# Kernel optimization log

Hardware: AMD Instinct MI355X
Metric: run time of the kernel (lower is better)

## Reference

```python
import jax, jax.numpy as jnp
import numpy as np
from jax import lax

B, CM, CQ, CO, H, W, KS = 8, 64, 64, 64, 128, 128, 3
K = KS * KS  # 9 kernel taps, offset_group=1


def setup_inputs() -> dict:
    key = jax.random.key(0)
    k1, k2, k3, k4 = jax.random.split(key, 4)
    mem = jax.random.normal(k1, (B, CM, H, W), jnp.float32)
    que = jax.random.normal(k2, (B, CQ, H, W), jnp.float32)
    # conv_offset: Conv2d(CM+CQ -> 3*K, 3x3, pad=1, bias=True); small init so offsets are a few px
    w_off = jax.random.normal(k3, (3 * K, CM + CQ, KS, KS), jnp.float32) * 0.01
    b_off = jnp.zeros((3 * K,), jnp.float32)
    # deformable conv weight: [CO, CM, 3, 3], bias=False
    w_def = jax.random.normal(k4, (CO, CM, KS, KS), jnp.float32) * (1.0 / np.sqrt(CM * K))
    return {"mem": mem, "que": que, "w_off": w_off, "b_off": b_off, "w_def": w_def}


def _deform_conv2d(mem, offset, mask, w_def):
    """Deformable conv v2 (stride=1, pad=1, dil=1, groups=1, offset_group=1).
    mem: [B,C,H,W]; offset: [B,2K,H,W] (dy,dx pairs per tap); mask: [B,K,H,W]."""
    Bn, C, Hn, Wn = mem.shape
    Kn = w_def.shape[2] * w_def.shape[3]
    off = offset.reshape(Bn, Kn, 2, Hn, Wn)
    dy, dx = off[:, :, 0], off[:, :, 1]            # [B,K,H,W]
    kk = jnp.arange(Kn)
    ky = (kk // KS - 1).astype(jnp.float32)        # kernel tap offsets with pad=1, dil=1
    kx = (kk % KS - 1).astype(jnp.float32)
    gy = jnp.arange(Hn, dtype=jnp.float32)
    gx = jnp.arange(Wn, dtype=jnp.float32)
    py = gy[None, None, :, None] + ky[None, :, None, None] + dy   # sample y coords [B,K,H,W]
    px = gx[None, None, None, :] + kx[None, :, None, None] + dx   # sample x coords [B,K,H,W]
    y0 = jnp.floor(py)
    x0 = jnp.floor(px)
    fy = py - y0
    fx = px - x0
    b_idx = jnp.arange(Bn)[:, None, None, None]

    def corner(iy, ix, wgt):
        valid = (iy >= 0) & (iy < Hn) & (ix >= 0) & (ix < Wn)  # zero padding outside
        iyc = jnp.clip(iy.astype(jnp.int32), 0, Hn - 1)
        ixc = jnp.clip(ix.astype(jnp.int32), 0, Wn - 1)
        vals = mem[b_idx, :, iyc, ixc]             # gather -> [B,K,H,W,C]
        return vals * (wgt * valid)[..., None]

    sampled = (corner(y0, x0, (1 - fy) * (1 - fx))
               + corner(y0, x0 + 1, (1 - fy) * fx)
               + corner(y0 + 1, x0, fy * (1 - fx))
               + corner(y0 + 1, x0 + 1, fy * fx))
    sampled = sampled * mask[..., None]            # modulation (applied raw, as in source)
    w = w_def.reshape(w_def.shape[0], C, Kn)       # [O,C,K]; tap order kh*KS+kw matches kk
    return jnp.einsum('bkhwc,ock->bohw', sampled, w)


def reference(mem, que, w_off, b_off, w_def):
    x = jnp.concatenate([mem, que], axis=1)
    off = lax.conv_general_dilated(
        x, w_off, window_strides=(1, 1), padding=[(1, 1), (1, 1)],
        dimension_numbers=('NCHW', 'OIHW', 'NCHW')) + b_off[None, :, None, None]
    offset, mask = off[:, :2 * K], off[:, 2 * K:]
    return _deform_conv2d(mem, offset, mask, w_def)
```

## Files before the change

kernel.cpp:

```cpp
#include <hip/hip_runtime.h>
#include <hip/hip_bf16.h>

#define Bn   8
#define CM_  64
#define CIN  128
#define CO_  64
#define Hn   128
#define Wn   128
#define Kn   9
#define COFF 27
#define HW   (Hn * Wn)

typedef __attribute__((ext_vector_type(8))) short bf16x8;
typedef __attribute__((ext_vector_type(4))) float f32x4;

__device__ __forceinline__ unsigned short f2bf(float x) {
    union { float f; unsigned u; } v; v.f = x;
    unsigned r = v.u + 0x7FFF + ((v.u >> 16) & 1);
    return (unsigned short)(r >> 16);
}
__device__ __forceinline__ float blo(unsigned u) {
    union { unsigned u; float f; } v; v.u = u << 16; return v.f;
}
__device__ __forceinline__ float bhi(unsigned u) {
    union { unsigned u; float f; } v; v.u = u & 0xffff0000u; return v.f;
}

__global__ __launch_bounds__(256) void transpose_kernel(
    const float* __restrict__ mem, const float* __restrict__ que,
    uint4* __restrict__ xT4)
{
    __shared__ unsigned tile[64 * 65];

    const int bb   = blockIdx.x & 7;
    const int pix0 = (blockIdx.x >> 3) * 64;
    const int tid  = threadIdx.x;
    const int pxL  = tid & 63;
    const int cg   = tid >> 6;

    const float* mb = mem + (size_t)bb * CM_ * HW + pix0 + pxL;
    const float* qb = que + (size_t)bb * CM_ * HW + pix0 + pxL;

    #pragma unroll
    for (int i = 0; i < 16; ++i) {
        const int c = cg * 32 + 2 * i;
        const float v0 = (c < CM_) ? mb[(size_t)c * HW]       : qb[(size_t)(c - CM_) * HW];
        const float v1 = (c + 1 < CM_) ? mb[(size_t)(c + 1) * HW] : qb[(size_t)(c + 1 - CM_) * HW];
        tile[pxL * 65 + cg * 16 + i] =
            (unsigned)f2bf(v0) | ((unsigned)f2bf(v1) << 16);
    }
    __syncthreads();

    uint4* dst = xT4 + (size_t)(bb * HW + pix0) * 16;
    #pragma unroll
    for (int p = 0; p < 4; ++p) {
        const int G  = p * 256 + tid;
        const int px = G >> 4;
        const int u  = G & 15;
        uint4 v;
        v.x = tile[px * 65 + u * 4 + 0];
        v.y = tile[px * 65 + u * 4 + 1];
        v.z = tile[px * 65 + u * 4 + 2];
        v.w = tile[px * 65 + u * 4 + 3];
        dst[G] = v;
    }
}

__global__ __launch_bounds__(256) void wprep_def_kernel(
    const float* __restrict__ w_def, unsigned short* __restrict__ wp)
{
    const int idx = blockIdx.x * 256 + threadIdx.x;
    if (idx >= CO_ * CM_ * Kn) return;
    const int j  = idx & 7;
    const int L  = (idx >> 3) & 63;
    const int f  = (idx >> 9) & 1;
    const int gk = idx >> 10;
    const int k  = gk % 9;
    const int g  = gk / 9;
    const int o  = g * 16 + (L & 15);
    const int c  = f * 32 + (L >> 4) * 8 + j;
    wp[idx] = f2bf(w_def[(size_t)(o * CM_ + c) * Kn + k]);
}

__global__ __launch_bounds__(256) void wprep_off_kernel(
    const float* __restrict__ w_off, unsigned short* __restrict__ wp)
{
    const int idx = blockIdx.x * 256 + threadIdx.x;
    if (idx >= 2 * 9 * 4 * 64 * 8) return;
    const int j   = idx & 7;
    const int L   = (idx >> 3) & 63;
    const int s   = (idx >> 9) & 3;
    const int r   = idx >> 11;
    const int tap = r % 9;
    const int ot  = r / 9;
    const int o   = ot * 16 + (L & 15);
    const int c   = s * 32 + (L >> 4) * 8 + j;
    wp[idx] = (o < COFF) ? f2bf(w_off[(size_t)(o * CIN + c) * Kn + tap]) : (unsigned short)0;
}

__global__ __launch_bounds__(256) void off_conv_mfma(
    const uint4* __restrict__ xT4, const uint4* __restrict__ wpo,
    const float* __restrict__ b_off, float* __restrict__ off)
{
    __shared__ uint4 xw[198 * 16];

    const int bb   = blockIdx.x & 7;
    const int pix0 = (blockIdx.x >> 3) * 64;
    const int h    = pix0 >> 7;
    const int w0   = pix0 & 127;
    const int tid  = threadIdx.x;
    const int wv   = tid >> 6;
    const int lane = tid & 63;
    const int quad = lane >> 4;
    const int lrow = lane & 15;
    const int ot   = wv >> 1;
    const int sub0 = (wv & 1) * 2;

    const uint4* xb = xT4 + (size_t)bb * HW * 16;

    #pragma unroll
    for (int g = 0; g < 13; ++g) {
        const int idx = g * 256 + tid;
        if (idx < 198 * 16) {
            const int slot = idx >> 4;
            const int j    = idx & 15;
            const int r    = slot / 66;
            const int c    = slot - r * 66;
            const int y    = h + r - 1;
            const int x    = w0 + c - 1;
            const bool ok  = (y >= 0) & (y < Hn) & (x >= 0) & (x < Wn);
            uint4 v = make_uint4(0, 0, 0, 0);
            if (ok) v = xb[(size_t)(y * Wn + x) * 16 + j];
            xw[slot * 16 + (j ^ (slot & 7))] = v;
        }
    }
    __syncthreads();

    f32x4 acc[2];
    #pragma unroll
    for (int t = 0; t < 2; ++t)
        #pragma unroll
        for (int r = 0; r < 4; ++r) {
            const int o = ot * 16 + quad * 4 + r;
            acc[t][r] = (o < COFF) ? b_off[o] : 0.0f;
        }

    #pragma unroll
    for (int tap = 0; tap < 9; ++tap) {
        const int rr = tap / 3;
        const int cc = tap % 3;

        const uint4* ap = wpo + (size_t)((ot * 9 + tap) * 4) * 64 + lane;
        bf16x8 a[4];
        #pragma unroll
        for (int s = 0; s < 4; ++s) a[s] = __builtin_bit_cast(bf16x8, ap[s * 64]);

        #pragma unroll
        for (int t = 0; t < 2; ++t) {
            const int pl   = (sub0 + t) * 16 + lrow;
            const int slot = rr * 66 + pl + cc;
            const int base = slot * 16;
            const int sw   = slot & 7;
            #pragma unroll
            for (int s = 0; s < 4; ++s) {
                const bf16x8 bfrag = __builtin_bit_cast(bf16x8,
                    xw[base + ((s * 4 + quad) ^ sw)]);
                acc[t] = __builtin_amdgcn_mfma_f32_16x16x32_bf16(
                    a[s], bfrag, acc[t], 0, 0, 0);
            }
        }
    }

    #pragma unroll
    for (int t = 0; t < 2; ++t) {
        const int pp = pix0 + (sub0 + t) * 16 + lrow;
        #pragma unroll
        for (int r = 0; r < 4; ++r) {
            const int o = ot * 16 + quad * 4 + r;
            if (o < COFF)
                off[(size_t)(bb * COFF + o) * HW + pp] = acc[t][r];
        }
    }
}

__global__ __launch_bounds__(256) void deform_mfma_kernel(
    const uint4* __restrict__ xT4, const float* __restrict__ off,
    const uint4* __restrict__ wprep, float* __restrict__ out)
{
    __shared__ uint4 smp4[64 * 8];

    const int bb    = blockIdx.x & 7;
    const int pix0  = (blockIdx.x >> 3) * 64;
    const int tid   = threadIdx.x;
    const int wv    = tid >> 6;
    const int lane  = tid & 63;
    const int quad  = lane >> 4;
    const int lrow  = lane & 15;
    const int chunk = lane & 7;
    const int psub  = lane >> 3;

    const uint4*  xb      = xT4 + (size_t)bb * HW * 16;
    const float*  offbase = off + (size_t)bb * COFF * HW;

    f32x4 acc[4];
    #pragma unroll
    for (int i = 0; i < 4; ++i) acc[i] = (f32x4){0.f, 0.f, 0.f, 0.f};

    for (int k = 0; k < Kn; ++k) {
        #pragma unroll
        for (int g = 0; g < 2; ++g) {
            const int pl = g * 32 + wv * 8 + psub;
            const int p  = pix0 + pl;
            const int h  = p >> 7;
            const int w  = p & 127;

            const float dy = offbase[(2 * k    ) * HW + p];
            const float dx = offbase[(2 * k + 1) * HW + p];
            const float mk = offbase[(18 + k   ) * HW + p];

            const float py = (float)(h + k / 3 - 1) + dy;
            const float px = (float)(w + k % 3 - 1) + dx;
            const float y0f = floorf(py), x0f = floorf(px);
            const float fy = py - y0f,  fx = px - x0f;
            const int y0 = (int)y0f, x0 = (int)x0f;
            const int y1 = y0 + 1,   x1 = x0 + 1;
            const bool vy0 = (y0 >= 0) & (y0 < Hn);
            const bool vy1 = (y1 >= 0) & (y1 < Hn);
            const bool vx0 = (x0 >= 0) & (x0 < Wn);
            const bool vx1 = (x1 >= 0) & (x1 < Wn);
            const float w00 = (1.f - fy) * (1.f - fx) * (float)(vy0 & vx0) * mk;
            const float w01 = (1.f - fy) * fx         * (float)(vy0 & vx1) * mk;
            const float w10 = fy * (1.f - fx)         * (float)(vy1 & vx0) * mk;
            const float w11 = fy * fx                 * (float)(vy1 & vx1) * mk;
            const int y0c = min(max(y0, 0), Hn - 1);
            const int y1c = min(max(y1, 0), Hn - 1);
            const int x0c = min(max(x0, 0), Wn - 1);
            const int x1c = min(max(x1, 0), Wn - 1);
            const int i00 = y0c * Wn + x0c, i01 = y0c * Wn + x1c;
            const int i10 = y1c * Wn + x0c, i11 = y1c * Wn + x1c;

            const uint4 v00 = xb[(size_t)i00 * 16 + chunk];
            const uint4 v01 = xb[(size_t)i01 * 16 + chunk];
            const uint4 v10 = xb[(size_t)i10 * 16 + chunk];
            const uint4 v11 = xb[(size_t)i11 * 16 + chunk];
            const unsigned u00[4] = {v00.x, v00.y, v00.z, v00.w};
            const unsigned u01[4] = {v01.x, v01.y, v01.z, v01.w};
            const unsigned u10[4] = {v10.x, v10.y, v10.z, v10.w};
            const unsigned u11[4] = {v11.x, v11.y, v11.z, v11.w};
            unsigned pk[4];
            #pragma unroll
            for (int d = 0; d < 4; ++d) {
                const float slo = w00 * blo(u00[d]) + w01 * blo(u01[d])
                                + w10 * blo(u10[d]) + w11 * blo(u11[d]);
                const float shi = w00 * bhi(u00[d]) + w01 * bhi(u01[d])
                                + w10 * bhi(u10[d]) + w11 * bhi(u11[d]);
                pk[d] = (unsigned)f2bf(slo) | ((unsigned)f2bf(shi) << 16);
            }
            smp4[pl * 8 + (chunk ^ (pl & 7))] =
                make_uint4(pk[0], pk[1], pk[2], pk[3]);
        }
        __syncthreads();

        const uint4* wpk = wprep + (size_t)((wv * 9 + k) * 2) * 64 + lane;
        const bf16x8 a0 = __builtin_bit_cast(bf16x8, wpk[0]);
        const bf16x8 a1 = __builtin_bit_cast(bf16x8, wpk[64]);

        #pragma unroll
        for (int nt = 0; nt < 4; ++nt) {
            const int pm = nt * 16 + lrow;
            const bf16x8 b0 = __builtin_bit_cast(bf16x8,
                smp4[pm * 8 + ( quad      ^ (pm & 7))]);
            const bf16x8 b1 = __builtin_bit_cast(bf16x8,
                smp4[pm * 8 + ((quad + 4) ^ (pm & 7))]);
            acc[nt] = __builtin_amdgcn_mfma_f32_16x16x32_bf16(a0, b0, acc[nt], 0, 0, 0);
            acc[nt] = __builtin_amdgcn_mfma_f32_16x16x32_bf16(a1, b1, acc[nt], 0, 0, 0);
        }
        __syncthreads();
    }

    const int obase = (wv << 4) + (quad << 2);
    #pragma unroll
    for (int nt = 0; nt < 4; ++nt) {
        const int pp = pix0 + nt * 16 + lrow;
        #pragma unroll
        for (int r = 0; r < 4; ++r)
            out[(size_t)(bb * CO_ + obase + r) * HW + pp] = acc[nt][r];
    }
}

extern "C" void kernel_launch(void* const* d_in, const int* in_sizes, int n_in,
                              void* d_out, int out_size, void* d_ws, size_t ws_size,
                              hipStream_t stream) {
    const float* mem   = (const float*)d_in[0];
    const float* que   = (const float*)d_in[1];
    const float* w_off = (const float*)d_in[2];
    const float* b_off = (const float*)d_in[3];
    const float* w_def = (const float*)d_in[4];
    float* out = (float*)d_out;

    char* ws = (char*)d_ws;
    float*          off  = (float*)ws;
    unsigned short* wpd  = (unsigned short*)(ws + 14155776);
    unsigned short* wpo  = (unsigned short*)(ws + 14229504);
    uint4*          xT4  = (uint4*)(ws + 14303232);

    transpose_kernel<<<2048, 256, 0, stream>>>(mem, que, xT4);
    wprep_def_kernel<<<144, 256, 0, stream>>>(w_def, wpd);
    wprep_off_kernel<<<144, 256, 0, stream>>>(w_off, wpo);
    off_conv_mfma<<<2048, 256, 0, stream>>>(xT4, (const uint4*)wpo, b_off, off);
    deform_mfma_kernel<<<2048, 256, 0, stream>>>(xT4, off, (const uint4*)wpd, out);
}
```

Measured before the change: 195.3 us.

## Double-buffer sample tile, prefetch next tap gathers, share offset math via shuffles

Doubles the shared sampling tile so the next tap's gathers are issued before the current tap's MFMAs, and the blend and write happen afterwards into the alternate buffer. This removes one barrier per tap and hides gather latency behind matrix work. Per-pixel offset and bilinear weight math is now done once per lane and broadcast with shuffles instead of being recomputed by all 8 chunk lanes. The blend uses packed float2 math and a library bf16x2 conversion. In exchange, register pressure rises from holding the prefetched gathers, and shared memory use doubles.

```diff
diff --git a/kernel.cpp b/kernel.cpp
--- a/kernel.cpp
+++ b/kernel.cpp
@@ -13,6 +13,7 @@
 
 typedef __attribute__((ext_vector_type(8))) short bf16x8;
 typedef __attribute__((ext_vector_type(4))) float f32x4;
+typedef __attribute__((ext_vector_type(2))) float f32x2;
 
 __device__ __forceinline__ unsigned short f2bf(float x) {
     union { float f; unsigned u; } v; v.f = x;
@@ -24,6 +25,12 @@
 }
 __device__ __forceinline__ float bhi(unsigned u) {
     union { unsigned u; float f; } v; v.u = u & 0xffff0000u; return v.f;
+}
+__device__ __forceinline__ unsigned pack_bf2(float lo, float hi) {
+    __hip_bfloat162 r = __float22bfloat162_rn(make_float2(lo, hi));
+    unsigned u;
+    __builtin_memcpy(&u, &r, 4);
+    return u;
 }
 
 __global__ __launch_bounds__(256) void transpose_kernel(
@@ -187,7 +194,7 @@
     const uint4* __restrict__ xT4, const float* __restrict__ off,
     const uint4* __restrict__ wprep, float* __restrict__ out)
 {
-    __shared__ uint4 smp4[64 * 8];
+    __shared__ uint4 smp4[2][64 * 8];
 
     const int bb    = blockIdx.x & 7;
     const int pix0  = (blockIdx.x >> 3) * 64;
@@ -202,64 +209,93 @@
     const uint4*  xb      = xT4 + (size_t)bb * HW * 16;
     const float*  offbase = off + (size_t)bb * COFF * HW;
 
+    const int pM = pix0 + lane;
+    const int hM = pM >> 7;
+    const int wM = pM & 127;
+
     f32x4 acc[4];
     #pragma unroll
     for (int i = 0; i < 4; ++i) acc[i] = (f32x4){0.f, 0.f, 0.f, 0.f};
 
-    for (int k = 0; k < Kn; ++k) {
+    float W00[2], W01[2], W10[2], W11[2];
+    uint4 G00[2], G01[2], G10[2], G11[2];
+
+    auto prep = [&](int k) {
+        const float dy = offbase[(2 * k    ) * HW + pM];
+        const float dx = offbase[(2 * k + 1) * HW + pM];
+        const float mk = offbase[(18 + k   ) * HW + pM];
+        const float py = (float)(hM + k / 3 - 1) + dy;
+        const float px = (float)(wM + k % 3 - 1) + dx;
+        const float y0f = floorf(py), x0f = floorf(px);
+        const float fy = py - y0f,  fx = px - x0f;
+        const int y0 = (int)y0f, x0 = (int)x0f;
+        const int y1 = y0 + 1,   x1 = x0 + 1;
+        const bool vy0 = (y0 >= 0) & (y0 < Hn);
+        const bool vy1 = (y1 >= 0) & (y1 < Hn);
+        const bool vx0 = (x0 >= 0) & (x0 < Wn);
+        const bool vx1 = (x1 >= 0) & (x1 < Wn);
+        const float w00 = (1.f - fy) * (1.f - fx) * (float)(vy0 & vx0) * mk;
+        const float w01 = (1.f - fy) * fx         * (float)(vy0 & vx1) * mk;
+        const float w10 = fy * (1.f - fx)         * (float)(vy1 & vx0) * mk;
+        const float w11 = fy * fx                 * (float)(vy1 & vx1) * mk;
+        const int y0c = min(max(y0, 0), Hn - 1);
+        const int y1c = min(max(y1, 0), Hn - 1);
+        const int x0c = min(max(x0, 0), Wn - 1);
+        const int x1c = min(max(x1, 0), Wn - 1);
+        const int i00 = y0c * Wn + x0c, i01 = y0c * Wn + x1c;
+        const int i10 = y1c * Wn + x0c, i11 = y1c * Wn + x1c;
+
         #pragma unroll
         for (int g = 0; g < 2; ++g) {
             const int pl = g * 32 + wv * 8 + psub;
-            const int p  = pix0 + pl;
-            const int h  = p >> 7;
-            const int w  = p & 127;
-
-            const float dy = offbase[(2 * k    ) * HW + p];
-            const float dx = offbase[(2 * k + 1) * HW + p];
-            const float mk = offbase[(18 + k   ) * HW + p];
-
-            const float py = (float)(h + k / 3 - 1) + dy;
-            const float px = (float)(w + k % 3 - 1) + dx;
-            const float y0f = floorf(py), x0f = floorf(px);
-            const float fy = py - y0f,  fx = px - x0f;
-            const int y0 = (int)y0f, x0 = (int)x0f;
-            const int y1 = y0 + 1,   x1 = x0 + 1;
-            const bool vy0 = (y0 >= 0) & (y0 < Hn);
-            const bool vy1 = (y1 >= 0) & (y1 < Hn);
-            const bool vx0 = (x0 >= 0) & (x0 < Wn);
-            const bool vx1 = (x1 >= 0) & (x1 < Wn);
-            const float w00 = (1.f - fy) * (1.f - fx) * (float)(vy0 & vx0) * mk;
-            const float w01 = (1.f - fy) * fx         * (float)(vy0 & vx1) * mk;
-            const float w10 = fy * (1.f - fx)         * (float)(vy1 & vx0) * mk;
-            const float w11 = fy * fx                 * (float)(vy1 & vx1) * mk;
-            const int y0c = min(max(y0, 0), Hn - 1);
-            const int y1c = min(max(y1, 0), Hn - 1);
-            const int x0c = min(max(x0, 0), Wn - 1);
-            const int x1c = min(max(x1, 0), Wn - 1);
-            const int i00 = y0c * Wn + x0c, i01 = y0c * Wn + x1c;
-            const int i10 = y1c * Wn + x0c, i11 = y1c * Wn + x1c;
-
-            const uint4 v00 = xb[(size_t)i00 * 16 + chunk];
-            const uint4 v01 = xb[(size_t)i01 * 16 + chunk];
-            const uint4 v10 = xb[(size_t)i10 * 16 + chunk];
-            const uint4 v11 = xb[(size_t)i11 * 16 + chunk];
-            const unsigned u00[4] = {v00.x, v00.y, v00.z, v00.w};
-            const unsigned u01[4] = {v01.x, v01.y, v01.z, v01.w};
-            const unsigned u10[4] = {v10.x, v10.y, v10.z, v10.w};
-            const unsigned u11[4] = {v11.x, v11.y, v11.z, v11.w};
+            W00[g] = __shfl(w00, pl, 64);
+            W01[g] = __shfl(w01, pl, 64);
+            W10[g] = __shfl(w10, pl, 64);
+            W11[g] = __shfl(w11, pl, 64);
+            const int I00 = __shfl(i00, pl, 64);
+            const int I01 = __shfl(i01, pl, 64);
+            const int I10 = __shfl(i10, pl, 64);
+            const int I11 = __shfl(i11, pl, 64);
+            G00[g] = xb[(size_t)I00 * 16 + chunk];
+            G01[g] = xb[(size_t)I01 * 16 + chunk];
+            G10[g] = xb[(size_t)I10 * 16 + chunk];
+            G11[g] = xb[(size_t)I11 * 16 + chunk];
+        }
+    };
+
+    auto blendwrite = [&](int buf) {
+        #pragma unroll
+        for (int g = 0; g < 2; ++g) {
+            const int pl = g * 32 + wv * 8 + psub;
+            const unsigned u00[4] = {G00[g].x, G00[g].y, G00[g].z, G00[g].w};
+            const unsigned u01[4] = {G01[g].x, G01[g].y, G01[g].z, G01[g].w};
+            const unsigned u10[4] = {G10[g].x, G10[g].y, G10[g].z, G10[g].w};
+            const unsigned u11[4] = {G11[g].x, G11[g].y, G11[g].z, G11[g].w};
             unsigned pk[4];
             #pragma unroll
             for (int d = 0; d < 4; ++d) {
-                const float slo = w00 * blo(u00[d]) + w01 * blo(u01[d])
-                                + w10 * blo(u10[d]) + w11 * blo(u11[d]);
-                const float shi = w00 * bhi(u00[d]) + w01 * bhi(u01[d])
-                                + w10 * bhi(u10[d]) + w11 * bhi(u11[d]);
-                pk[d] = (unsigned)f2bf(slo) | ((unsigned)f2bf(shi) << 16);
+                const f32x2 c00 = {blo(u00[d]), bhi(u00[d])};
+                const f32x2 c01 = {blo(u01[d]), bhi(u01[d])};
+                const f32x2 c10 = {blo(u10[d]), bhi(u10[d])};
+                const f32x2 c11 = {blo(u11[d]), bhi(u11[d])};
+                const f32x2 s = W00[g] * c00 + W01[g] * c01
+                              + W10[g] * c10 + W11[g] * c11;
+                pk[d] = pack_bf2(s.x, s.y);
             }
-            smp4[pl * 8 + (chunk ^ (pl & 7))] =
+            smp4[buf][pl * 8 + (chunk ^ (pl & 7))] =
                 make_uint4(pk[0], pk[1], pk[2], pk[3]);
         }
-        __syncthreads();
+    };
+
+    prep(0);
+    blendwrite(0);
+    __syncthreads();
+
+    #pragma unroll
+    for (int k = 0; k < Kn; ++k) {
+        const int cur = k & 1;
+
+        if (k < Kn - 1) prep(k + 1);
 
         const uint4* wpk = wprep + (size_t)((wv * 9 + k) * 2) * 64 + lane;
         const bf16x8 a0 = __builtin_bit_cast(bf16x8, wpk[0]);
@@ -269,12 +305,14 @@
         for (int nt = 0; nt < 4; ++nt) {
             const int pm = nt * 16 + lrow;
             const bf16x8 b0 = __builtin_bit_cast(bf16x8,
-                smp4[pm * 8 + ( quad      ^ (pm & 7))]);
+                smp4[cur][pm * 8 + ( quad      ^ (pm & 7))]);
             const bf16x8 b1 = __builtin_bit_cast(bf16x8,
-                smp4[pm * 8 + ((quad + 4) ^ (pm & 7))]);
+                smp4[cur][pm * 8 + ((quad + 4) ^ (pm & 7))]);
             acc[nt] = __builtin_amdgcn_mfma_f32_16x16x32_bf16(a0, b0, acc[nt], 0, 0, 0);
             acc[nt] = __builtin_amdgcn_mfma_f32_16x16x32_bf16(a1, b1, acc[nt], 0, 0, 0);
         }
+
+        if (k < Kn - 1) blendwrite(cur ^ 1);
         __syncthreads();
     }
 
```

Result: faster. 185.9 us (-4.8%).
